# Optimization experiments

Hardware: AMD Instinct MI355X
Metric: run time of the kernel (lower is better)

## Reference

```python
import jax, jax.numpy as jnp
import numpy as np

B_SZ = 32; CTX = 8192; NP = 512; P = 16          # batch, context, n_patches, patch_size
DM = 1024; DS = 16; DC = 4; EXP = 2               # d_model, d_state, d_conv, expand
DI = EXP * DM                                     # d_inner = 2048
DTR = DM // 16                                    # dt_rank = 64


def _ln(x, g, b, eps=1e-5):
    m = x.mean(-1, keepdims=True)
    v = ((x - m) ** 2).mean(-1, keepdims=True)
    return (x - m) / jnp.sqrt(v + eps) * g + b


def _posemb_sincos_1d(n, d, temperature=10000.0):
    pos = jnp.arange(n, dtype=jnp.float32)
    omega = jnp.arange(d // 2, dtype=jnp.float32) / (d // 2 - 1)
    omega = 1.0 / (temperature ** omega)
    ang = pos[:, None] * omega[None, :]            # [n, d/2]
    return jnp.concatenate([jnp.sin(ang), jnp.cos(ang)], axis=1)  # [n, d]


def setup_inputs() -> dict:
    key = jax.random.key(0)
    ks = jax.random.split(key, 10)
    s = lambda k, shape, scale: jax.random.normal(k, shape, jnp.float32) * scale
    return {
        "x": jax.random.normal(ks[0], (B_SZ, CTX), jnp.float32),
        # patch embedding: LN(patch) -> Linear(P, DM) -> LN(DM)
        "ln1_g": jnp.ones((P,), jnp.float32), "ln1_b": jnp.zeros((P,), jnp.float32),
        "Wp": s(ks[1], (P, DM), P ** -0.5), "bp": jnp.zeros((DM,), jnp.float32),
        "ln2_g": jnp.ones((DM,), jnp.float32), "ln2_b": jnp.zeros((DM,), jnp.float32),
        # Mamba block params (mamba-ssm conventions: in_proj/out_proj bias=False, conv bias=True)
        "W_in": s(ks[2], (DM, 2 * DI), DM ** -0.5),
        "conv_w": s(ks[3], (DI, DC), DC ** -0.5), "conv_b": jnp.zeros((DI,), jnp.float32),
        "W_x": s(ks[4], (DI, DTR + 2 * DS), DI ** -0.5),
        "W_dt": s(ks[5], (DTR, DI), DTR ** -0.5),
        "b_dt": jnp.full((DI,), -4.6, jnp.float32),  # softplus(b_dt) ~ 0.01 (typical dt init)
        "A_log": jnp.log(jnp.broadcast_to(jnp.arange(1, DS + 1, dtype=jnp.float32), (DI, DS))),
        "D": jnp.ones((DI,), jnp.float32),
        "W_out": s(ks[6], (DI, DM), DI ** -0.5),
        "ln3_g": jnp.ones((DM,), jnp.float32), "ln3_b": jnp.zeros((DM,), jnp.float32),
        "Wh": s(ks[7], (DM, 1), DM ** -0.5), "bh": jnp.zeros((1,), jnp.float32),
    }


def reference(x, ln1_g, ln1_b, Wp, bp, ln2_g, ln2_b, W_in, conv_w, conv_b,
              W_x, W_dt, b_dt, A_log, D, W_out, ln3_g, ln3_b, Wh, bh):
    B = x.shape[0]
    # --- patch embedding: 'b 1 (n p) -> b n p' (c=1), LN, Linear, LN ---
    patches = x.reshape(B, NP, P)
    h = _ln(patches, ln1_g, ln1_b)
    h = h @ Wp + bp
    h = _ln(h, ln2_g, ln2_b)                        # [B, NP, DM]
    h = h + _posemb_sincos_1d(NP, DM)
    # --- Mamba block ---
    xz = h @ W_in                                   # [B, NP, 2*DI]
    u, z = jnp.split(xz, 2, axis=-1)                # [B, NP, DI] each
    # causal depthwise conv1d (kernel DC, left-padded), then SiLU
    up = jnp.pad(u, ((0, 0), (DC - 1, 0), (0, 0)))
    uc = sum(up[:, k:k + NP, :] * conv_w[:, k] for k in range(DC)) + conv_b
    uc = jax.nn.silu(uc)
    # input-dependent SSM params
    xd = uc @ W_x                                   # [B, NP, DTR+2*DS]
    dt, Bm, Cm = jnp.split(xd, [DTR, DTR + DS], axis=-1)
    delta = jax.nn.softplus(dt @ W_dt + b_dt)       # [B, NP, DI]
    A = -jnp.exp(A_log)                             # [DI, DS]

    def step(hstate, inps):
        d_t, B_t, C_t, u_t = inps                   # [B,DI], [B,DS], [B,DS], [B,DI]
        dA = jnp.exp(d_t[..., None] * A)            # [B, DI, DS]
        hstate = hstate * dA + (d_t * u_t)[..., None] * B_t[:, None, :]
        y_t = jnp.einsum('bdn,bn->bd', hstate, C_t)
        return hstate, y_t

    h0 = jnp.zeros((B, DI, DS), x.dtype)
    xs = (delta.transpose(1, 0, 2), Bm.transpose(1, 0, 2),
          Cm.transpose(1, 0, 2), uc.transpose(1, 0, 2))
    _, ys = jax.lax.scan(step, h0, xs)              # ys: [NP, B, DI]
    y = ys.transpose(1, 0, 2) + uc * D              # skip connection D*u
    y = y * jax.nn.silu(z)                          # gate
    y = y @ W_out                                   # [B, NP, DM]
    pooled = y.mean(axis=1)                         # [B, DM]
    out = (_ln(pooled, ln3_g, ln3_b) @ Wh + bh).squeeze()  # [B]
    return out
```

## Files before the change

kernel.cpp:

```cpp
#include <hip/hip_runtime.h>
#include <hip/hip_bf16.h>

#define BSZ  32
#define CTX  8192
#define NP_  512
#define PSZ  16
#define DM_  1024
#define DS_  16
#define DI_  2048
#define DTR_ 64
#define NTOK (BSZ*NP_)

typedef __hip_bfloat16 bf16;
typedef short bf16x8 __attribute__((ext_vector_type(8)));
typedef float f32x4  __attribute__((ext_vector_type(4)));

typedef __attribute__((address_space(3))) void lds_t;
typedef __attribute__((address_space(1))) void gbl_t;

__device__ inline float bf2f(bf16 v){ return __bfloat162float(v); }
__device__ inline bf16  f2bf(float v){ return __float2bfloat16(v); }
__device__ inline float bfs2f(short s){ union{unsigned u; float f;} x; x.u = ((unsigned)(unsigned short)s)<<16; return x.f; }
__device__ inline short f2bfs(float v){ bf16 b = f2bf(v); return *reinterpret_cast<short*>(&b); }
__device__ inline float fast_sigmoid(float x){ return 1.0f/(1.0f+__expf(-x)); }
__device__ inline void stout(float* p, float v){ *p = v; }
__device__ inline void stout(bf16* p, float v){ *p = f2bf(v); }
__device__ inline float hw_exp2(float x){ float r; asm("v_exp_f32 %0, %1" : "=v"(r) : "v"(x)); return r; }
__device__ inline float hw_log2(float x){ float r; asm("v_log_f32 %0, %1" : "=v"(r) : "v"(x)); return r; }
__device__ inline float softplus_fast(float x){
  if (x > 15.0f) return x;
  return 0.69314718f * hw_log2(1.0f + hw_exp2(x * 1.44269504f));
}

__device__ inline void gload_lds16(const void* g, void* l){
  __builtin_amdgcn_global_load_lds((const gbl_t*)g, (lds_t*)l, 16, 0, 0);
}

__device__ inline void transpose_cvt_body(
    int bx, int by, const float* __restrict__ W, bf16* __restrict__ T,
    int ldw, int col0, int nvalid, int K, int tid, float (*tile)[65])
{
  int kb = bx << 6, nb = by << 6;
  int c = tid & 63, r4 = tid >> 6;
  #pragma unroll
  for (int i=0;i<16;i++){
    int r = r4 + i*4;
    int kk = kb + r, nn = nb + c;
    float v = 0.f;
    if (kk < K && nn < nvalid) v = W[(size_t)kk*ldw + col0 + nn];
    tile[r][c] = v;
  }
  __syncthreads();
  #pragma unroll
  for (int i=0;i<16;i++){
    int r = r4 + i*4;
    T[(size_t)(nb + r)*K + kb + c] = f2bf(tile[c][r]);
  }
}

__global__ __launch_bounds__(256) void k_prep_all(
    const float* __restrict__ W_in, bf16* __restrict__ winT,
    const float* __restrict__ W_x,  bf16* __restrict__ wxT,
    const float* __restrict__ W_dt, bf16* __restrict__ wdtT,
    float* __restrict__ pe,
    const float* __restrict__ cw, float* __restrict__ cwT)
{
  __shared__ float tile[64][65];
  int b = blockIdx.x, tid = threadIdx.x;
  if (b < 1024){
    transpose_cvt_body(b & 15, b >> 4, W_in, winT, 4096, 0, 4096, 1024, tid, tile);
  } else if (b < 1088){
    int t = b - 1024;
    transpose_cvt_body(t & 31, t >> 5, W_x, wxT, 96, 0, 96, 2048, tid, tile);
  } else if (b < 1120){
    int t = b - 1088;
    transpose_cvt_body(0, t, W_dt, wdtT, 2048, 0, 2048, 64, tid, tile);
  } else if (b < 3168){
    int idx = (b - 1120)*256 + tid;
    int n = idx >> 10, c = idx & 1023;
    int j2 = c & 511;
    float omega = exp2f(-13.2877123795495f * ((float)j2 * (1.0f/511.0f)));
    float ang = (float)n * omega;
    pe[idx] = (c < 512) ? sinf(ang) : cosf(ang);
  } else {
    int idx = (b - 3168)*256 + tid;
    int k = idx >> 11, d = idx & 2047;
    cwT[idx] = cw[d*4 + k];
  }
}

__global__ __launch_bounds__(256) void k_patch(
    const float* __restrict__ x, const float* __restrict__ g1, const float* __restrict__ b1,
    const float* __restrict__ Wp, const float* __restrict__ bp,
    const float* __restrict__ g2, const float* __restrict__ b2,
    const float* __restrict__ pe, bf16* __restrict__ h)
{
  __shared__ float pns[2][16];
  __shared__ float red[8];
  int tid = threadIdx.x;
  int w = tid >> 6, l = tid & 63;
  int tok0 = blockIdx.x << 4;
  int bb = tok0 >> 9, n0 = tok0 & 511;
  float wreg[4][16];
  #pragma unroll
  for (int q=0;q<4;q++)
    #pragma unroll
    for (int i=0;i<16;i++)
      wreg[q][i] = Wp[i*1024 + tid + q*256];
  float bpv[4], g2v[4], b2v[4];
  #pragma unroll
  for (int q=0;q<4;q++){
    int j = tid + q*256;
    bpv[q] = bp[j]; g2v[q] = g2[j]; b2v[q] = b2[j];
  }
  float g1v = 0.f, b1v = 0.f;
  if (tid < 16){ g1v = g1[tid]; b1v = b1[tid]; }
  for (int tt=0; tt<16; ++tt){
    int buf = tt & 1;
    if (tid < 16){
      float v = x[(size_t)bb*CTX + (n0+tt)*16 + tid];
      float m = v;
      #pragma unroll
      for (int o=1;o<16;o<<=1) m += __shfl_xor(m, o, 64);
      m *= (1.0f/16.0f);
      float dv = v - m;
      float s = dv*dv;
      #pragma unroll
      for (int o=1;o<16;o<<=1) s += __shfl_xor(s, o, 64);
      float rs = rsqrtf(s*(1.0f/16.0f) + 1e-5f);
      pns[buf][tid] = dv*rs*g1v + b1v;
    }
    __syncthreads();
    float acc[4];
    #pragma unroll
    for (int q=0;q<4;q++) acc[q] = bpv[q];
    #pragma unroll
    for (int i=0;i<16;i++){
      float p = pns[buf][i];
      #pragma unroll
      for (int q=0;q<4;q++) acc[q] += p*wreg[q][i];
    }
    float s1 = acc[0]+acc[1]+acc[2]+acc[3];
    float s2 = acc[0]*acc[0]+acc[1]*acc[1]+acc[2]*acc[2]+acc[3]*acc[3];
    #pragma unroll
    for (int o=32;o;o>>=1){ s1 += __shfl_down(s1,o,64); s2 += __shfl_down(s2,o,64); }
    if (l==0){ red[w]=s1; red[4+w]=s2; }
    __syncthreads();
    float mu  = (red[0]+red[1]+red[2]+red[3])*(1.0f/1024.0f);
    float var = (red[4]+red[5]+red[6]+red[7])*(1.0f/1024.0f) - mu*mu;
    float rs2 = rsqrtf(var + 1e-5f);
    size_t tok = (size_t)(tok0 + tt);
    #pragma unroll
    for (int q=0;q<4;q++){
      int j = tid + q*256;
      float val = (acc[q]-mu)*rs2*g2v[q] + b2v[q] + pe[(n0+tt)*1024 + j];
      h[tok*1024 + j] = f2bf(val);
    }
  }
}

__global__ __launch_bounds__(512, 2) void k_gemm256(
    const bf16* __restrict__ A, const bf16* __restrict__ BT,
    bf16* __restrict__ Cu, bf16* __restrict__ Cz, int M, int N, int K)
{
  __shared__ __align__(16) bf16 As[2][256*64];
  __shared__ __align__(16) bf16 Bs[2][256*64];
  const int tid = threadIdx.x;
  const int w = tid >> 6, l = tid & 63, lr = l & 15, lg = l >> 4;
  const int wm = w >> 2, wn = w & 3;
  int nblk = N >> 8;
  int nwg = gridDim.x;
  int wg  = (blockIdx.x & 7) * (nwg >> 3) + (blockIdx.x >> 3);
  const int GM = 4;
  int band = GM * nblk;
  int grp = wg / band, loc = wg % band;
  int bm = grp*GM + (loc % GM);
  int bn = loc / GM;
  int m0 = bm << 8, n0 = bn << 8;

  f32x4 acc[8][4] = {};

  int rowS[4], colS[4];
  #pragma unroll
  for (int j=0;j<4;j++){
    int bo = (j*8 + w)*1024 + l*16;
    int r = bo >> 7;
    int c = (bo & 127) ^ ((r & 7) << 4);
    rowS[j] = r; colS[j] = c >> 1;
  }
  const bf16* Ag = A  + (size_t)m0 * K;
  const bf16* Bg = BT + (size_t)n0 * K;

  #define STAGE(buf, kt) do {                                                   \
    _Pragma("unroll")                                                           \
    for (int j=0;j<4;j++)                                                       \
      gload_lds16(Ag + (size_t)rowS[j]*K + (kt) + colS[j], &As[buf][(j*8+w)*512]); \
    _Pragma("unroll")                                                           \
    for (int j=0;j<4;j++)                                                       \
      gload_lds16(Bg + (size_t)rowS[j]*K + (kt) + colS[j], &Bs[buf][(j*8+w)*512]); \
  } while(0)

  int cswz[2];
  cswz[0] = (lg*8) ^ ((lr&7)<<3);
  cswz[1] = (32 + lg*8) ^ ((lr&7)<<3);
  const int rbA = (wm*128 + lr) * 64;
  const int rbB = (wn*64  + lr) * 64;

  #define COMPUTE(buf) do {                                                     \
    _Pragma("unroll")                                                           \
    for (int kk=0;kk<2;kk++){                                                   \
      bf16x8 bq[4];                                                             \
      _Pragma("unroll")                                                         \
      for (int j=0;j<4;j++) bq[j] = *(const bf16x8*)&Bs[buf][rbB + j*1024 + cswz[kk]]; \
      _Pragma("unroll")                                                         \
      for (int rh=0;rh<2;rh++){                                                 \
        bf16x8 af[4];                                                           \
        _Pragma("unroll")                                                       \
        for (int i=0;i<4;i++) af[i] = *(const bf16x8*)&As[buf][rbA + (rh*4+i)*1024 + cswz[kk]]; \
        __builtin_amdgcn_s_setprio(1);                                          \
        _Pragma("unroll")                                                       \
        for (int i=0;i<4;i++)                                                   \
          _Pragma("unroll")                                                     \
          for (int j=0;j<4;j++)                                                 \
            acc[rh*4+i][j] = __builtin_amdgcn_mfma_f32_16x16x32_bf16(af[i], bq[j], acc[rh*4+i][j], 0,0,0); \
        __builtin_amdgcn_s_setprio(0);                                          \
      }                                                                         \
    }                                                                           \
  } while(0)

  STAGE(0, 0);
  STAGE(1, 64);
  const int NT2 = K >> 7;
  int kt = 0;
  for (int t=0; t<NT2; ++t){
    const bool last = (t == NT2-1);
    asm volatile("s_waitcnt vmcnt(8)" ::: "memory");
    __builtin_amdgcn_sched_barrier(0);
    asm volatile("s_barrier" ::: "memory");
    COMPUTE(0);
    asm volatile("s_barrier" ::: "memory");
    __builtin_amdgcn_sched_barrier(0);
    if (!last) STAGE(0, kt + 128);
    if (!last) { asm volatile("s_waitcnt vmcnt(8)" ::: "memory"); }
    else       { asm volatile("s_waitcnt vmcnt(0)" ::: "memory"); }
    __builtin_amdgcn_sched_barrier(0);
    asm volatile("s_barrier" ::: "memory");
    COMPUTE(1);
    if (!last){
      asm volatile("s_barrier" ::: "memory");
      __builtin_amdgcn_sched_barrier(0);
      STAGE(1, kt + 192);
    }
    kt += 128;
  }
  #undef STAGE
  #undef COMPUTE

  #pragma unroll
  for (int fr=0;fr<8;fr++)
    #pragma unroll
    for (int fc=0;fc<4;fc++)
      #pragma unroll
      for (int rr=0;rr<4;rr++){
        int row  = m0 + wm*128 + fr*16 + lg*4 + rr;
        int gcol = n0 + wn*64 + fc*16 + lr;
        float v = acc[fr][fc][rr];
        if (gcol < 2048) Cu[(size_t)row*2048 + gcol] = f2bf(v);
        else { v = v * fast_sigmoid(v); Cz[(size_t)row*2048 + gcol - 2048] = f2bf(v); }
      }
}

template<int EPI, typename OT>
__global__ __launch_bounds__(256) void k_gemm_bt(
    const bf16* __restrict__ A, const bf16* __restrict__ BT, OT* __restrict__ C,
    bf16* __restrict__ C2, int M, int N, int K, const float* __restrict__ bias)
{
  __shared__ __align__(16) bf16 As[128*32];
  __shared__ __align__(16) bf16 Bs[128*32];
  int tid = threadIdx.x;
  int mblk = M >> 7, nblk = N >> 7;
  int nwg = gridDim.x;
  int wg  = (blockIdx.x & 7) * (nwg >> 3) + (blockIdx.x >> 3);
  const int GM = 8;
  int band = GM * nblk;
  int grp = wg / band, loc = wg % band;
  int bm = grp*GM + (loc % GM);
  int bn = loc / GM;
  int m0 = bm << 7, n0 = bn << 7;
  int w = tid >> 6, l = tid & 63, lr = l & 15, lg = l >> 4;
  int wm = w >> 1, wn = w & 1;
  f32x4 acc[4][4] = {};
  int r0 = tid >> 2, c0 = (tid & 3) << 3;
  const bf16* Asrc = A  + (size_t)(m0 + r0) * K + c0;
  const bf16* Bsrc = BT + (size_t)(n0 + r0) * K + c0;
  bf16* AsW = As + w*512;
  bf16* BsW = Bs + w*512;
  for (int kt = 0; kt < K; kt += 32){
    __syncthreads();
    gload_lds16(Asrc + kt,                   AsW);
    gload_lds16(Asrc + (size_t)64*K + kt,    AsW + 2048);
    gload_lds16(Bsrc + kt,                   BsW);
    gload_lds16(Bsrc + (size_t)64*K + kt,    BsW + 2048);
    __syncthreads();
    bf16x8 af[4], bfr[4];
    #pragma unroll
    for (int i=0;i<4;i++) af[i]  = *(const bf16x8*)(As + (wm*64 + i*16 + lr)*32 + lg*8);
    #pragma unroll
    for (int j=0;j<4;j++) bfr[j] = *(const bf16x8*)(Bs + (wn*64 + j*16 + lr)*32 + lg*8);
    #pragma unroll
    for (int i=0;i<4;i++)
      #pragma unroll
      for (int j=0;j<4;j++)
        acc[i][j] = __builtin_amdgcn_mfma_f32_16x16x32_bf16(af[i], bfr[j], acc[i][j], 0,0,0);
  }
  #pragma unroll
  for (int i=0;i<4;i++)
    #pragma unroll
    for (int j=0;j<4;j++)
      #pragma unroll
      for (int r=0;r<4;r++){
        int row = m0 + wm*64 + i*16 + lg*4 + r;
        int col = wn*64 + j*16 + lr;
        int gcol = n0 + col;
        float v = acc[i][j][r];
        if (EPI == 0) stout(&C[(size_t)row*N + gcol], v);
        if (EPI == 1){ v = softplus_fast(v + bias[gcol]); stout(&C[(size_t)row*N + gcol], v); }
      }
}

__global__ __launch_bounds__(256) void k_gemm_xk(
    const bf16* __restrict__ A, const bf16* __restrict__ BT,
    float* __restrict__ C0, float* __restrict__ C1,
    float* __restrict__ C2, float* __restrict__ C3)
{
  __shared__ __align__(16) bf16 As[128*32];
  __shared__ __align__(16) bf16 Bs[128*32];
  int tid = threadIdx.x;
  int nwg = gridDim.x;
  int wg  = (blockIdx.x & 7) * (nwg >> 3) + (blockIdx.x >> 3);
  int chunk = wg >> 7;
  int bm = wg & 127;
  int m0 = bm << 7;
  int kbase = chunk << 9;
  int w = tid >> 6, l = tid & 63, lr = l & 15, lg = l >> 4;
  int wm = w >> 1, wn = w & 1;
  f32x4 acc[4][4] = {};
  int r0 = tid >> 2, c0 = (tid & 3) << 3;
  const bf16* Asrc = A  + (size_t)(m0 + r0) * 2048 + kbase + c0;
  const bf16* Bsrc = BT + (size_t)r0 * 2048 + kbase + c0;
  bf16* AsW = As + w*512;
  bf16* BsW = Bs + w*512;
  float* Cp = (chunk==0) ? C0 : (chunk==1) ? C1 : (chunk==2) ? C2 : C3;
  for (int kt = 0; kt < 512; kt += 32){
    __syncthreads();
    gload_lds16(Asrc + kt,                      AsW);
    gload_lds16(Asrc + (size_t)64*2048 + kt,    AsW + 2048);
    gload_lds16(Bsrc + kt,                      BsW);
    gload_lds16(Bsrc + (size_t)64*2048 + kt,    BsW + 2048);
    __syncthreads();
    bf16x8 af[4], bfr[4];
    #pragma unroll
    for (int i=0;i<4;i++) af[i]  = *(const bf16x8*)(As + (wm*64 + i*16 + lr)*32 + lg*8);
    #pragma unroll
    for (int j=0;j<4;j++) bfr[j] = *(const bf16x8*)(Bs + (wn*64 + j*16 + lr)*32 + lg*8);
    #pragma unroll
    for (int i=0;i<4;i++)
      #pragma unroll
      for (int j=0;j<4;j++)
        acc[i][j] = __builtin_amdgcn_mfma_f32_16x16x32_bf16(af[i], bfr[j], acc[i][j], 0,0,0);
  }
  #pragma unroll
  for (int i=0;i<4;i++)
    #pragma unroll
    for (int j=0;j<4;j++)
      #pragma unroll
      for (int r=0;r<4;r++){
        int row = m0 + wm*64 + i*16 + lg*4 + r;
        int gcol = wn*64 + j*16 + lr;
        Cp[(size_t)row*128 + gcol] = acc[i][j][r];
      }
}

__global__ __launch_bounds__(256) void k_xproj_fix(
    float* __restrict__ xd, const float* __restrict__ p1,
    const float* __restrict__ p2, const float* __restrict__ p3,
    bf16* __restrict__ dt)
{
  int idx = blockIdx.x*256 + threadIdx.x;
  int row = idx >> 7, col = idx & 127;
  float v = xd[idx] + p1[idx] + p2[idx] + p3[idx];
  xd[idx] = v;
  if (col < 64) dt[(row << 6) + col] = f2bf(v);
}

__global__ __launch_bounds__(256) void k_conv(
    const bf16* __restrict__ u, const float* __restrict__ cwT, const float* __restrict__ cb,
    bf16* __restrict__ uc)
{
  int tid = threadIdx.x;
  int d = tid << 3;
  int tok0 = blockIdx.x << 4;
  int n0 = tok0 & 511;
  float wk[4][8];
  #pragma unroll
  for (int k=0;k<4;k++){
    *(float4*)&wk[k][0] = *(const float4*)(cwT + k*2048 + d);
    *(float4*)&wk[k][4] = *(const float4*)(cwT + k*2048 + d + 4);
  }
  float cbv[8];
  *(float4*)&cbv[0] = *(const float4*)(cb + d);
  *(float4*)&cbv[4] = *(const float4*)(cb + d + 4);
  bf16x8 w0, w1, w2;
  if (n0 == 0){
    w0 = (bf16x8){0,0,0,0,0,0,0,0}; w1 = w0; w2 = w0;
  } else {
    w0 = *(const bf16x8*)(u + (size_t)(tok0-3)*2048 + d);
    w1 = *(const bf16x8*)(u + (size_t)(tok0-2)*2048 + d);
    w2 = *(const bf16x8*)(u + (size_t)(tok0-1)*2048 + d);
  }
  #pragma unroll 4
  for (int t=0; t<16; ++t){
    size_t tok = (size_t)(tok0 + t);
    bf16x8 cur = *(const bf16x8*)(u + tok*2048 + d);
    bf16x8 res;
    #pragma unroll
    for (int j=0;j<8;j++){
      float a = cbv[j]
              + wk[0][j]*bfs2f(w0[j]) + wk[1][j]*bfs2f(w1[j])
              + wk[2][j]*bfs2f(w2[j]) + wk[3][j]*bfs2f(cur[j]);
      res[j] = f2bfs(a * fast_sigmoid(a));
    }
    *(bf16x8*)(uc + tok*2048 + d) = res;
    w0 = w1; w1 = w2; w2 = cur;
  }
}

__global__ __launch_bounds__(256) void k_scan(
    const bf16* __restrict__ delta, const bf16* __restrict__ uc, const bf16* __restrict__ g,
    const float* __restrict__ xd, const float* __restrict__ A_log,
    const float* __restrict__ Dp, float* __restrict__ ysum)
{
  int tid = threadIdx.x;
  int q  = tid & 3;
  int dl = tid >> 2;
  int b  = blockIdx.x >> 5;
  int d  = ((blockIdx.x & 31) << 6) + dl;
  const float L2E = 1.44269504f;
  float4 t4 = *(const float4*)(A_log + (size_t)d*16 + q*4);
  float An0 = -__expf(t4.x)*L2E, An1 = -__expf(t4.y)*L2E,
        An2 = -__expf(t4.z)*L2E, An3 = -__expf(t4.w)*L2E;
  float Dd = (q == 0) ? Dp[d] : 0.0f;
  float h0=0.f,h1=0.f,h2=0.f,h3=0.f;
  float acc = 0.0f;
  unsigned o1 = (unsigned)b*1048576u + (unsigned)d;
  unsigned o2 = (unsigned)b*16384u + 16u + (unsigned)q;
  const float4* __restrict__ x4 = (const float4*)xd;
  #pragma unroll 4
  for (int t=0; t<512; ++t){
    float dt = bf2f(delta[o1]);
    float ut = bf2f(uc[o1]);
    float gt = bf2f(g[o1]);
    float4 Bq = x4[o2];
    float4 Cq = x4[o2 + 4u];
    o1 += 2048u; o2 += 32u;
    float du = dt*ut;
    float y;
    float e0 = hw_exp2(dt*An0); h0 = h0*e0 + du*Bq.x; y  = h0*Cq.x;
    float e1 = hw_exp2(dt*An1); h1 = h1*e1 + du*Bq.y; y += h1*Cq.y;
    float e2 = hw_exp2(dt*An2); h2 = h2*e2 + du*Bq.z; y += h2*Cq.z;
    float e3 = hw_exp2(dt*An3); h3 = h3*e3 + du*Bq.w; y += h3*Cq.w;
    acc += (y + ut*Dd) * gt;
  }
  acc += __shfl_xor(acc, 1, 64);
  acc += __shfl_xor(acc, 2, 64);
  if (q == 0) ysum[(size_t)b*2048 + d] = acc;
}

__global__ __launch_bounds__(256) void k_poolgemm_part(
    const float* __restrict__ ysum, const float* __restrict__ Wo, float* __restrict__ partial)
{
  __shared__ float ys[32][64];
  int tid = threadIdx.x;
  int jb = blockIdx.x & 15;
  int kc = blockIdx.x >> 4;
  int j  = jb*64 + (tid & 63);
  int b0 = tid >> 6;
  #pragma unroll
  for (int i=0;i<8;i++){
    int e = tid + i*256;
    int bb = e >> 6, kk = e & 63;
    ys[bb][kk] = ysum[(size_t)bb*2048 + kc*64 + kk];
  }
  __syncthreads();
  float acc[8];
  #pragma unroll
  for (int p=0;p<8;p++) acc[p] = 0.f;
  #pragma unroll 4
  for (int kk=0;kk<64;kk++){
    float wv = Wo[(size_t)(kc*64 + kk)*1024 + j];
    #pragma unroll
    for (int p=0;p<8;p++) acc[p] += ys[b0*8 + p][kk] * wv;
  }
  #pragma unroll
  for (int p=0;p<8;p++)
    partial[((size_t)kc*32 + b0*8 + p)*1024 + j] = acc[p];
}

__global__ __launch_bounds__(256) void k_pool_reduce(
    const float* __restrict__ partial, float* __restrict__ pooled)
{
  int idx = blockIdx.x*256 + threadIdx.x;
  float s = 0.f;
  #pragma unroll 8
  for (int kc=0;kc<32;kc++) s += partial[(size_t)kc*32768 + idx];
  pooled[idx] = s * (1.0f/512.0f);
}

__global__ __launch_bounds__(256) void k_head(
    const float* __restrict__ pooled, const float* __restrict__ g, const float* __restrict__ bb,
    const float* __restrict__ Wh, const float* __restrict__ bh, float* __restrict__ out)
{
  __shared__ float red[8];
  int b = blockIdx.x, tid = threadIdx.x;
  float v[4];
  #pragma unroll
  for (int q=0;q<4;q++) v[q] = pooled[(size_t)b*1024 + tid + q*256];
  float s1 = v[0]+v[1]+v[2]+v[3];
  float s2 = v[0]*v[0]+v[1]*v[1]+v[2]*v[2]+v[3]*v[3];
  #pragma unroll
  for (int o=32;o;o>>=1){ s1 += __shfl_down(s1,o,64); s2 += __shfl_down(s2,o,64); }
  int w = tid>>6, l = tid&63;
  if (l==0){ red[w]=s1; red[4+w]=s2; }
  __syncthreads();
  float mu  = (red[0]+red[1]+red[2]+red[3])*(1.0f/1024.0f);
  float var = (red[4]+red[5]+red[6]+red[7])*(1.0f/1024.0f) - mu*mu;
  float rs = rsqrtf(var + 1e-5f);
  float p = 0.f;
  #pragma unroll
  for (int q=0;q<4;q++){
    int jv = tid + q*256;
    p += ((v[q]-mu)*rs*g[jv] + bb[jv]) * Wh[jv];
  }
  #pragma unroll
  for (int o=32;o;o>>=1) p += __shfl_down(p,o,64);
  __syncthreads();
  if (l==0) red[w] = p;
  __syncthreads();
  if (tid==0) out[b] = red[0]+red[1]+red[2]+red[3] + bh[0];
}

extern "C" void kernel_launch(void* const* d_in, const int* in_sizes, int n_in,
                              void* d_out, int out_size, void* d_ws, size_t ws_size,
                              hipStream_t stream)
{
  const float* x     = (const float*)d_in[0];
  const float* ln1_g = (const float*)d_in[1];
  const float* ln1_b = (const float*)d_in[2];
  const float* Wp    = (const float*)d_in[3];
  const float* bp    = (const float*)d_in[4];
  const float* ln2_g = (const float*)d_in[5];
  const float* ln2_b = (const float*)d_in[6];
  const float* W_in  = (const float*)d_in[7];
  const float* conv_w= (const float*)d_in[8];
  const float* conv_b= (const float*)d_in[9];
  const float* W_x   = (const float*)d_in[10];
  const float* W_dt  = (const float*)d_in[11];
  const float* b_dt  = (const float*)d_in[12];
  const float* A_log = (const float*)d_in[13];
  const float* Dv    = (const float*)d_in[14];
  const float* W_out = (const float*)d_in[15];
  const float* ln3_g = (const float*)d_in[16];
  const float* ln3_b = (const float*)d_in[17];
  const float* Wh    = (const float*)d_in[18];
  const float* bh    = (const float*)d_in[19];

  char* ws = (char*)d_ws;
  size_t o = 0;
  bf16*  u_delta = (bf16*)(ws + o); o += (size_t)NTOK*DI_*2;
  bf16*  zbuf    = (bf16*)(ws + o); o += (size_t)NTOK*DI_*2;
  bf16*  ucbuf   = (bf16*)(ws + o); o += (size_t)NTOK*DI_*2;
  char*  poolA   = (ws + o);        o += (size_t)NTOK*DM_*2;
  bf16*  winT    = (bf16*)(ws + o); o += (size_t)2*DI_*DM_*2;
  float* pe      = (float*)(ws + o); o += (size_t)NP_*DM_*4;
  bf16*  wxT     = (bf16*)(ws + o); o += (size_t)128*2048*2;
  bf16*  wdtT    = (bf16*)(ws + o); o += (size_t)2048*64*2;
  float* cwT     = (float*)(ws + o); o += (size_t)4*2048*4;
  bf16*  hbuf    = (bf16*)poolA;
  float* xdbuf   = (float*)(poolA + 0);
  bf16*  dtbuf   = (bf16*) (poolA + 8388608);
  float* ysumbuf = (float*)(poolA + 11272192);
  float* pooledb = (float*)(poolA + 11534336);
  float* partial = (float*)(poolA + 12582912);
  float* xpart1  = (float*)winT;
  float* xpart2  = (float*)u_delta;
  float* xpart3  = (float*)((char*)u_delta + 8388608);

  k_prep_all      <<<3200, 256, 0, stream>>>(W_in, winT, W_x, wxT, W_dt, wdtT, pe, conv_w, cwT);
  k_patch         <<<1024, 256, 0, stream>>>(x, ln1_g, ln1_b, Wp, bp, ln2_g, ln2_b, pe, hbuf);
  k_gemm256       <<<1024, 512, 0, stream>>>(hbuf, winT, u_delta, zbuf, NTOK, 4096, 1024);
  k_conv          <<<1024, 256, 0, stream>>>(u_delta, cwT, conv_b, ucbuf);
  k_gemm_xk       <<<512,  256, 0, stream>>>(ucbuf, wxT, xdbuf, xpart1, xpart2, xpart3);
  k_xproj_fix     <<<8192, 256, 0, stream>>>(xdbuf, xpart1, xpart2, xpart3, dtbuf);
  k_gemm_bt<1,bf16><<<2048,256, 0, stream>>>(dtbuf, wdtT, u_delta, nullptr, NTOK, 2048, 64, b_dt);
  k_scan          <<<1024, 256, 0, stream>>>(u_delta, ucbuf, zbuf, xdbuf, A_log, Dv, ysumbuf);
  k_poolgemm_part <<<512,  256, 0, stream>>>(ysumbuf, W_out, partial);
  k_pool_reduce   <<<128,  256, 0, stream>>>(partial, pooledb);
  k_head          <<<32,   256, 0, stream>>>(pooledb, ln3_g, ln3_b, Wh, bh, (float*)d_out);
  (void)in_sizes; (void)n_in; (void)out_size; (void)ws_size;
}
```

Measured before the change: 476.8 us.

## Split selective scan into two time halves with linear correction pass

The scan over 512 timesteps is split into two independent halves run by separate blocks, doubling the grid. The second half starts from zero state and tracks the cumulative decay product P and a gated C-weighted sum M, so the missing contribution of the first half's final state can be added later as dot(hmid, M). A small fix kernel combines both partial sums with this correction. This shortens the serial dependency chain and raises occupancy, in exchange for extra per-step multiplies, an additional launch and some scratch traffic.

```diff
diff --git a/kernel.cpp b/kernel.cpp
--- a/kernel.cpp
+++ b/kernel.cpp
@@ -438,13 +438,16 @@
 __global__ __launch_bounds__(256) void k_scan(
     const bf16* __restrict__ delta, const bf16* __restrict__ uc, const bf16* __restrict__ g,
     const float* __restrict__ xd, const float* __restrict__ A_log,
-    const float* __restrict__ Dp, float* __restrict__ ysum)
+    const float* __restrict__ Dp, float* __restrict__ hmid,
+    float* __restrict__ Mbuf, float* __restrict__ pacc)
 {
   int tid = threadIdx.x;
   int q  = tid & 3;
   int dl = tid >> 2;
-  int b  = blockIdx.x >> 5;
-  int d  = ((blockIdx.x & 31) << 6) + dl;
+  int bx = blockIdx.x;
+  int b    = bx >> 6;
+  int half = (bx >> 5) & 1;
+  int d  = ((bx & 31) << 6) + dl;
   const float L2E = 1.44269504f;
   float4 t4 = *(const float4*)(A_log + (size_t)d*16 + q*4);
   float An0 = -__expf(t4.x)*L2E, An1 = -__expf(t4.y)*L2E,
@@ -452,28 +455,68 @@
   float Dd = (q == 0) ? Dp[d] : 0.0f;
   float h0=0.f,h1=0.f,h2=0.f,h3=0.f;
   float acc = 0.0f;
-  unsigned o1 = (unsigned)b*1048576u + (unsigned)d;
-  unsigned o2 = (unsigned)b*16384u + 16u + (unsigned)q;
+  unsigned o1 = (unsigned)b*1048576u + (unsigned)half*524288u + (unsigned)d;
+  unsigned o2 = (unsigned)b*16384u + (unsigned)half*8192u + 16u + (unsigned)q;
   const float4* __restrict__ x4 = (const float4*)xd;
-  #pragma unroll 4
-  for (int t=0; t<512; ++t){
-    float dt = bf2f(delta[o1]);
-    float ut = bf2f(uc[o1]);
-    float gt = bf2f(g[o1]);
-    float4 Bq = x4[o2];
-    float4 Cq = x4[o2 + 4u];
-    o1 += 2048u; o2 += 32u;
-    float du = dt*ut;
-    float y;
-    float e0 = hw_exp2(dt*An0); h0 = h0*e0 + du*Bq.x; y  = h0*Cq.x;
-    float e1 = hw_exp2(dt*An1); h1 = h1*e1 + du*Bq.y; y += h1*Cq.y;
-    float e2 = hw_exp2(dt*An2); h2 = h2*e2 + du*Bq.z; y += h2*Cq.z;
-    float e3 = hw_exp2(dt*An3); h3 = h3*e3 + du*Bq.w; y += h3*Cq.w;
-    acc += (y + ut*Dd) * gt;
+  size_t sidx = ((size_t)b*2048 + d)*16 + q*4;
+  if (half == 0){
+    #pragma unroll 4
+    for (int t=0; t<256; ++t){
+      float dt = bf2f(delta[o1]);
+      float ut = bf2f(uc[o1]);
+      float gt = bf2f(g[o1]);
+      float4 Bq = x4[o2];
+      float4 Cq = x4[o2 + 4u];
+      o1 += 2048u; o2 += 32u;
+      float du = dt*ut;
+      float y;
+      float e0 = hw_exp2(dt*An0); h0 = h0*e0 + du*Bq.x; y  = h0*Cq.x;
+      float e1 = hw_exp2(dt*An1); h1 = h1*e1 + du*Bq.y; y += h1*Cq.y;
+      float e2 = hw_exp2(dt*An2); h2 = h2*e2 + du*Bq.z; y += h2*Cq.z;
+      float e3 = hw_exp2(dt*An3); h3 = h3*e3 + du*Bq.w; y += h3*Cq.w;
+      acc += (y + ut*Dd) * gt;
+    }
+    *(float4*)(hmid + sidx) = make_float4(h0, h1, h2, h3);
+  } else {
+    float P0=1.f,P1=1.f,P2=1.f,P3=1.f;
+    float M0=0.f,M1=0.f,M2=0.f,M3=0.f;
+    #pragma unroll 4
+    for (int t=0; t<256; ++t){
+      float dt = bf2f(delta[o1]);
+      float ut = bf2f(uc[o1]);
+      float gt = bf2f(g[o1]);
+      float4 Bq = x4[o2];
+      float4 Cq = x4[o2 + 4u];
+      o1 += 2048u; o2 += 32u;
+      float du = dt*ut;
+      float y;
+      float e0 = hw_exp2(dt*An0); h0 = h0*e0 + du*Bq.x; y  = h0*Cq.x; P0 *= e0; M0 = fmaf(gt, Cq.x*P0, M0);
+      float e1 = hw_exp2(dt*An1); h1 = h1*e1 + du*Bq.y; y += h1*Cq.y; P1 *= e1; M1 = fmaf(gt, Cq.y*P1, M1);
+      float e2 = hw_exp2(dt*An2); h2 = h2*e2 + du*Bq.z; y += h2*Cq.z; P2 *= e2; M2 = fmaf(gt, Cq.z*P2, M2);
+      float e3 = hw_exp2(dt*An3); h3 = h3*e3 + du*Bq.w; y += h3*Cq.w; P3 *= e3; M3 = fmaf(gt, Cq.w*P3, M3);
+      acc += (y + ut*Dd) * gt;
+    }
+    *(float4*)(Mbuf + sidx) = make_float4(M0, M1, M2, M3);
   }
   acc += __shfl_xor(acc, 1, 64);
   acc += __shfl_xor(acc, 2, 64);
-  if (q == 0) ysum[(size_t)b*2048 + d] = acc;
+  if (q == 0) pacc[(size_t)half*65536 + (size_t)b*2048 + d] = acc;
+}
+
+__global__ __launch_bounds__(256) void k_scan_fix(
+    const float* __restrict__ hmid, const float* __restrict__ Mbuf,
+    const float* __restrict__ pacc, float* __restrict__ ysum)
+{
+  int idx = blockIdx.x*256 + threadIdx.x;
+  const float4* H = (const float4*)(hmid + (size_t)idx*16);
+  const float4* M = (const float4*)(Mbuf + (size_t)idx*16);
+  float c = 0.f;
+  #pragma unroll
+  for (int i=0;i<4;i++){
+    float4 hh = H[i], mm = M[i];
+    c += hh.x*mm.x + hh.y*mm.y + hh.z*mm.z + hh.w*mm.w;
+  }
+  ysum[idx] = pacc[idx] + pacc[65536 + idx] + c;
 }
 
 __global__ __launch_bounds__(256) void k_poolgemm_part(
@@ -591,6 +634,9 @@
   float* ysumbuf = (float*)(poolA + 11272192);
   float* pooledb = (float*)(poolA + 11534336);
   float* partial = (float*)(poolA + 12582912);
+  float* hmid    = (float*)(poolA + 16777216);
+  float* Mbuf    = (float*)(poolA + 20971520);
+  float* paccb   = (float*)(poolA + 25165824);
   float* xpart1  = (float*)winT;
   float* xpart2  = (float*)u_delta;
   float* xpart3  = (float*)((char*)u_delta + 8388608);
@@ -602,7 +648,8 @@
   k_gemm_xk       <<<512,  256, 0, stream>>>(ucbuf, wxT, xdbuf, xpart1, xpart2, xpart3);
   k_xproj_fix     <<<8192, 256, 0, stream>>>(xdbuf, xpart1, xpart2, xpart3, dtbuf);
   k_gemm_bt<1,bf16><<<2048,256, 0, stream>>>(dtbuf, wdtT, u_delta, nullptr, NTOK, 2048, 64, b_dt);
-  k_scan          <<<1024, 256, 0, stream>>>(u_delta, ucbuf, zbuf, xdbuf, A_log, Dv, ysumbuf);
+  k_scan          <<<2048, 256, 0, stream>>>(u_delta, ucbuf, zbuf, xdbuf, A_log, Dv, hmid, Mbuf, paccb);
+  k_scan_fix      <<<256,  256, 0, stream>>>(hmid, Mbuf, paccb, ysumbuf);
   k_poolgemm_part <<<512,  256, 0, stream>>>(ysumbuf, W_out, partial);
   k_pool_reduce   <<<128,  256, 0, stream>>>(partial, pooledb);
   k_head          <<<32,   256, 0, stream>>>(pooledb, ln3_g, ln3_b, Wh, bh, (float*)d_out);
```

After: 509.3 us. 6.8% more time.
